# Performance work log

Measured on AMD Instinct MI355X. Metric: run time of the kernel, lower is better.

## Reference

```python
import jax, jax.numpy as jnp
from jax import lax
import numpy as np


def _farthest_point_sample(points, num_centroids):
    """points: [B, C, N] float. Returns int32 indices [B, num_centroids].

    Standard PointNet++ CUDA semantics: start from point index 0, maintain a
    running min squared distance to the selected set, pick argmax each step.
    """
    B, C, N = points.shape

    def step(carry, _):
        min_dist, farthest = carry  # [B, N], [B]
        # gather current centroid coords: [B, C, 1]
        centroid = jnp.take_along_axis(points, farthest[:, None, None], axis=2)
        d = jnp.sum((points - centroid) ** 2, axis=1)  # [B, N]
        min_dist = jnp.minimum(min_dist, d)
        nxt = jnp.argmax(min_dist, axis=1).astype(jnp.int32)  # [B]
        return (min_dist, nxt), farthest

    init = (jnp.full((B, N), jnp.finfo(points.dtype).max, points.dtype),
            jnp.zeros((B,), jnp.int32))
    _, idx = lax.scan(step, init, None, length=num_centroids)  # idx: [S, B]
    return idx.T  # [B, num_centroids]


def setup_inputs() -> dict:
    key = jax.random.key(0)
    B, C, N = 32, 3, 131072
    points = jax.random.normal(key, (B, C, N), dtype=jnp.float32)
    return {"points": points, "num_centroids": 2048}


def reference(points, num_centroids):
    return _farthest_point_sample(points, num_centroids)
```

## Files before the change

kernel.cpp:

```cpp
#include <hip/hip_runtime.h>
#include <stdint.h>

typedef unsigned long long u64;

#define NBATCH 32
#define NPTS   131072
#define KBLK   8
#define PPB    (NPTS / KBLK)
#define NTHR   1024
#define NWAVE  (NTHR / 64)
#define PPT    (PPB / NTHR)
#define FLT_MAX_C 3.402823466e+38f

__device__ __forceinline__ u64* slot_ptr(u64* slots, int b, int k, int par) {
    return slots + ((size_t)((b * KBLK + k) * 2 + par)) * 8;
}

__global__ __launch_bounds__(NTHR, 4)
void fps_kernel(const float* __restrict__ points, int* __restrict__ out,
                u64* __restrict__ slots, int S)
{
    const int b    = blockIdx.x & (NBATCH - 1);
    const int kk   = blockIdx.x >> 5;
    const int t    = threadIdx.x;
    const int lane = t & 63;
    const int wv   = t >> 6;

    const float* pb = points + (size_t)b * 3 * NPTS;
    const float* bx = pb + kk * PPB;
    const float* by = bx + NPTS;
    const float* bz = bx + 2 * NPTS;

    float px[PPT], py[PPT], pz[PPT], md[PPT];
    const int t4 = t * 4;
#pragma unroll
    for (int c = 0; c < PPT / 4; ++c) {
        float4 vx = *(const float4*)(bx + c * (NTHR * 4) + t4);
        float4 vy = *(const float4*)(by + c * (NTHR * 4) + t4);
        float4 vz = *(const float4*)(bz + c * (NTHR * 4) + t4);
        px[c*4+0]=vx.x; px[c*4+1]=vx.y; px[c*4+2]=vx.z; px[c*4+3]=vx.w;
        py[c*4+0]=vy.x; py[c*4+1]=vy.y; py[c*4+2]=vy.z; py[c*4+3]=vy.w;
        pz[c*4+0]=vz.x; pz[c*4+1]=vz.y; pz[c*4+2]=vz.z; pz[c*4+3]=vz.w;
        md[c*4+0]=FLT_MAX_C; md[c*4+1]=FLT_MAX_C;
        md[c*4+2]=FLT_MAX_C; md[c*4+3]=FLT_MAX_C;
    }

    __shared__ float s_v[NWAVE];
    __shared__ int   s_i[NWAVE];
    __shared__ int   s_bi;
    __shared__ unsigned s_bc[4];

    float cx = pb[0], cy = pb[NPTS], cz = pb[2 * NPTS];
    if (kk == 0 && t == 0) out[(size_t)b * S] = 0;

    for (int s = 1; s < S; ++s) {
        float bestv = -1.0f;
        int   bestp = 0;
#pragma unroll
        for (int p = 0; p < PPT; ++p) {
            float dx = __fsub_rn(px[p], cx);
            float dy = __fsub_rn(py[p], cy);
            float dz = __fsub_rn(pz[p], cz);
            float d  = __fadd_rn(__fadd_rn(__fmul_rn(dx, dx), __fmul_rn(dy, dy)),
                                 __fmul_rn(dz, dz));
            float m  = fminf(md[p], d);
            md[p] = m;
            bool tk = m > bestv;
            bestv = tk ? m : bestv;
            bestp = tk ? p : bestp;
        }
        int gidx = kk * PPB + (bestp >> 2) * (NTHR * 4) + t4 + (bestp & 3);

#pragma unroll
        for (int off = 32; off >= 1; off >>= 1) {
            float ov = __shfl_down(bestv, off);
            int   oi = __shfl_down(gidx, off);
            bool tk = (ov > bestv) || (ov == bestv && oi < gidx);
            bestv = tk ? ov : bestv;
            gidx  = tk ? oi : gidx;
        }
        if (lane == 0) { s_v[wv] = bestv; s_i[wv] = gidx; }
        __syncthreads();

        if (wv == 0) {
            float v16 = (lane < NWAVE) ? s_v[lane] : -1.0f;
            int   i16 = (lane < NWAVE) ? s_i[lane] : 0x7fffffff;
#pragma unroll
            for (int off = 8; off >= 1; off >>= 1) {
                float ov = __shfl_down(v16, off);
                int   oi = __shfl_down(i16, off);
                bool tk = (ov > v16) || (ov == v16 && oi < i16);
                v16 = tk ? ov : v16;
                i16 = tk ? oi : i16;
            }
            if (lane == 0) {
                u64 di = ((u64)(unsigned)s << 49)
                       | ((u64)__float_as_uint(v16) << 17)
                       | (u64)(unsigned)(131071 - i16);
                __hip_atomic_store(slot_ptr(slots, b, kk, s & 1) + 3, di,
                                   __ATOMIC_RELAXED, __HIP_MEMORY_SCOPE_AGENT);
                s_bi = i16;
            }
        }
        __syncthreads();

        int widx = s_bi;
        if ((widx >> 14) == kk) {
            int l = widx & (PPB - 1);
            if (t == ((l >> 2) & (NTHR - 1))) {
                int pw = ((l >> 12) << 2) | (l & 3);
                float wx = 0.f, wy = 0.f, wz = 0.f;
#pragma unroll
                for (int p = 0; p < PPT; ++p) {
                    bool e = (p == pw);
                    wx = e ? px[p] : wx; wy = e ? py[p] : wy; wz = e ? pz[p] : wz;
                }
                u64 tg = (u64)(unsigned)s << 32;
                u64* sp = slot_ptr(slots, b, kk, s & 1);
                __hip_atomic_store(sp + 0, tg | __float_as_uint(wx),
                                   __ATOMIC_RELAXED, __HIP_MEMORY_SCOPE_AGENT);
                __hip_atomic_store(sp + 1, tg | __float_as_uint(wy),
                                   __ATOMIC_RELAXED, __HIP_MEMORY_SCOPE_AGENT);
                __hip_atomic_store(sp + 2, tg | __float_as_uint(wz),
                                   __ATOMIC_RELAXED, __HIP_MEMORY_SCOPE_AGENT);
            }
        }

        if (wv == 0) {
            u64 got = 0;
            if (lane < 32) {
                u64* ps = slot_ptr(slots, b, lane >> 2, s & 1) + (lane & 3);
                const int sh = ((lane & 3) == 3) ? 49 : 32;
                do {
                    got = __hip_atomic_load(ps, __ATOMIC_RELAXED,
                                            __HIP_MEMORY_SCOPE_AGENT);
                } while ((int)(got >> sh) != s);
            }
            u64 dval = (u64)__shfl((long long)got, lane * 4 + 3);
            u64 dv = (lane < 8) ? dval : 0ull;
#pragma unroll
            for (int off = 4; off >= 1; off >>= 1) {
                u64 o = (u64)__shfl_down((long long)dv, off);
                dv = (o > dv) ? o : dv;
            }
            u64 win = (u64)__shfl((long long)dv, 0);
            u64 mask = __ballot(lane < 8 && dval == win);
            int w = __ffsll(mask) - 1;
            unsigned lo = (unsigned)got;
            unsigned cxb = (unsigned)__shfl((int)lo, w * 4 + 0);
            unsigned cyb = (unsigned)__shfl((int)lo, w * 4 + 1);
            unsigned czb = (unsigned)__shfl((int)lo, w * 4 + 2);
            int idx = 131071 - (int)(win & 0x1FFFF);
            if (lane == 0) {
                s_bc[0] = cxb; s_bc[1] = cyb; s_bc[2] = czb; s_bc[3] = (unsigned)idx;
                if (kk == 0) out[(size_t)b * S + s] = idx;
            }
        }
        __syncthreads();
        cx = __uint_as_float(s_bc[0]);
        cy = __uint_as_float(s_bc[1]);
        cz = __uint_as_float(s_bc[2]);
    }
}

extern "C" void kernel_launch(void* const* d_in, const int* in_sizes, int n_in,
                              void* d_out, int out_size, void* d_ws, size_t ws_size,
                              hipStream_t stream) {
    const float* points = (const float*)d_in[0];
    int* out   = (int*)d_out;
    u64* slots = (u64*)d_ws;
    int S = out_size / NBATCH;
    fps_kernel<<<dim3(NBATCH * KBLK), dim3(NTHR), 0, stream>>>(points, out, slots, S);
}
```

Before: 7.051 ms.

## Interleave two batches per block to hide cross-block sync latency

Each block now handles the same point slice for two batches (A and B), with the points split across 16 blocks per batch instead of 8. While one batch waits on the inter-block slot exchange, the block scans the other batch, and slot loads are prefetched ahead of polling. The goal is to hide the global-memory polling latency of the per-step all-to-all reduction. In exchange, register pressure stays similar per thread, each poll now covers 16 blocks, and the schedule becomes more intricate, including a tail step that finishes batch B alone.

Measured after the change: 10.42 ms. +47.8%, slower.

```diff
diff --git a/kernel.cpp b/kernel.cpp
--- a/kernel.cpp
+++ b/kernel.cpp
@@ -4,8 +4,9 @@
 typedef unsigned long long u64;
 
 #define NBATCH 32
+#define NPAIR  16
 #define NPTS   131072
-#define KBLK   8
+#define KBLK   16
 #define PPB    (NPTS / KBLK)
 #define NTHR   1024
 #define NWAVE  (NTHR / 64)
@@ -16,150 +17,230 @@
     return slots + ((size_t)((b * KBLK + k) * 2 + par)) * 8;
 }
 
+#define SCAN(PX,PY,PZ,MD,CX,CY,CZ,BV,GI) do {                                  \
+    float bv_ = -1.0f; int bp_ = 0;                                            \
+    _Pragma("unroll")                                                          \
+    for (int p = 0; p < PPT; ++p) {                                            \
+        float dx = __fsub_rn(PX[p], CX);                                       \
+        float dy = __fsub_rn(PY[p], CY);                                       \
+        float dz = __fsub_rn(PZ[p], CZ);                                       \
+        float d  = __fadd_rn(__fadd_rn(__fmul_rn(dx,dx), __fmul_rn(dy,dy)),    \
+                             __fmul_rn(dz,dz));                                \
+        float m  = fminf(MD[p], d);                                            \
+        MD[p] = m;                                                             \
+        bool tk = m > bv_;                                                     \
+        bv_ = tk ? m : bv_;                                                    \
+        bp_ = tk ? p : bp_;                                                    \
+    }                                                                          \
+    BV = bv_;                                                                  \
+    GI = kk * PPB + ((bp_ >> 2) * (NTHR * 4)) + t4 + (bp_ & 3);                \
+} while (0)
+
+#define REDPUB(PX,PY,PZ,BX,SS,BV,GI) do {                                      \
+    float bv_ = BV; int gi_ = GI;                                              \
+    _Pragma("unroll")                                                          \
+    for (int off = 32; off >= 1; off >>= 1) {                                  \
+        float ov = __shfl_down(bv_, off);                                      \
+        int   oi = __shfl_down(gi_, off);                                      \
+        bool tk = (ov > bv_) || (ov == bv_ && oi < gi_);                       \
+        bv_ = tk ? ov : bv_;                                                   \
+        gi_ = tk ? oi : gi_;                                                   \
+    }                                                                          \
+    if (lane == 0) { s_v[wv] = bv_; s_i[wv] = gi_; }                           \
+    __syncthreads();                                                           \
+    if (wv == 0) {                                                             \
+        float v16 = (lane < NWAVE) ? s_v[lane] : -1.0f;                        \
+        int   i16 = (lane < NWAVE) ? s_i[lane] : 0x7fffffff;                   \
+        _Pragma("unroll")                                                      \
+        for (int off = 8; off >= 1; off >>= 1) {                               \
+            float ov = __shfl_down(v16, off);                                  \
+            int   oi = __shfl_down(i16, off);                                  \
+            bool tk = (ov > v16) || (ov == v16 && oi < i16);                   \
+            v16 = tk ? ov : v16;                                               \
+            i16 = tk ? oi : i16;                                               \
+        }                                                                      \
+        if (lane == 0) {                                                       \
+            u64 di = ((u64)(unsigned)(SS) << 49)                               \
+                   | ((u64)__float_as_uint(v16) << 17)                         \
+                   | (u64)(unsigned)(131071 - i16);                            \
+            __hip_atomic_store(slot_ptr(slots, BX, kk, (SS) & 1) + 3, di,      \
+                               __ATOMIC_RELAXED, __HIP_MEMORY_SCOPE_AGENT);    \
+            s_bi = i16;                                                        \
+        }                                                                      \
+    }                                                                          \
+    __syncthreads();                                                           \
+    {                                                                          \
+        int widx = s_bi;                                                       \
+        if ((widx >> 13) == kk) {                                              \
+            int l = widx & (PPB - 1);                                          \
+            if (t == ((l >> 2) & (NTHR - 1))) {                                \
+                int pw = ((l >> 12) << 2) | (l & 3);                           \
+                float wx = 0.f, wy = 0.f, wz = 0.f;                            \
+                _Pragma("unroll")                                              \
+                for (int p = 0; p < PPT; ++p) {                                \
+                    bool e = (p == pw);                                        \
+                    wx = e ? PX[p] : wx;                                       \
+                    wy = e ? PY[p] : wy;                                       \
+                    wz = e ? PZ[p] : wz;                                       \
+                }                                                              \
+                u64 tg = (u64)(unsigned)(SS) << 32;                            \
+                u64* sp = slot_ptr(slots, BX, kk, (SS) & 1);                   \
+                __hip_atomic_store(sp + 0, tg | __float_as_uint(wx),           \
+                                   __ATOMIC_RELAXED, __HIP_MEMORY_SCOPE_AGENT);\
+                __hip_atomic_store(sp + 1, tg | __float_as_uint(wy),           \
+                                   __ATOMIC_RELAXED, __HIP_MEMORY_SCOPE_AGENT);\
+                __hip_atomic_store(sp + 2, tg | __float_as_uint(wz),           \
+                                   __ATOMIC_RELAXED, __HIP_MEMORY_SCOPE_AGENT);\
+            }                                                                  \
+        }                                                                      \
+    }                                                                          \
+} while (0)
+
+#define PREFETCH(BX, SS, PRE) do {                                             \
+    if (wv == 0) {                                                             \
+        u64* ps = slot_ptr(slots, BX, lane >> 2, (SS) & 1) + (lane & 3);       \
+        PRE = __hip_atomic_load(ps, __ATOMIC_RELAXED,                          \
+                                __HIP_MEMORY_SCOPE_AGENT);                     \
+    }                                                                          \
+} while (0)
+
+#define POLLSEL(BX, SS, PRE, SBC) do {                                         \
+    if (wv == 0) {                                                             \
+        u64* ps = slot_ptr(slots, BX, lane >> 2, (SS) & 1) + (lane & 3);       \
+        const int sh = ((lane & 3) == 3) ? 49 : 32;                            \
+        u64 got = PRE;                                                         \
+        while ((int)(got >> sh) != (SS))                                       \
+            got = __hip_atomic_load(ps, __ATOMIC_RELAXED,                      \
+                                    __HIP_MEMORY_SCOPE_AGENT);                 \
+        u64 dval = (u64)__shfl((long long)got, ((lane & 15) << 2) | 3);        \
+        u64 dv = (lane < 16) ? dval : 0ull;                                    \
+        _Pragma("unroll")                                                      \
+        for (int off = 8; off >= 1; off >>= 1) {                               \
+            u64 o = (u64)__shfl_down((long long)dv, off);                      \
+            dv = (o > dv) ? o : dv;                                            \
+        }                                                                      \
+        u64 win = (u64)__shfl((long long)dv, 0);                               \
+        u64 mask = __ballot(lane < 16 && dval == win);                         \
+        int w = __ffsll(mask) - 1;                                             \
+        unsigned lo = (unsigned)got;                                           \
+        unsigned cxb = (unsigned)__shfl((int)lo, (w << 2) | 0);                \
+        unsigned cyb = (unsigned)__shfl((int)lo, (w << 2) | 1);                \
+        unsigned czb = (unsigned)__shfl((int)lo, (w << 2) | 2);                \
+        int idx = 131071 - (int)(win & 0x1FFFF);                               \
+        if (lane == 0) {                                                       \
+            SBC[0] = cxb; SBC[1] = cyb; SBC[2] = czb;                          \
+            if (kk == 0) out[(size_t)(BX) * S + (SS)] = idx;                   \
+        }                                                                      \
+    }                                                                          \
+    __syncthreads();                                                           \
+} while (0)
+
 __global__ __launch_bounds__(NTHR, 4)
 void fps_kernel(const float* __restrict__ points, int* __restrict__ out,
                 u64* __restrict__ slots, int S)
 {
-    const int b    = blockIdx.x & (NBATCH - 1);
-    const int kk   = blockIdx.x >> 5;
+    const int pr   = blockIdx.x & (NPAIR - 1);
+    const int kk   = blockIdx.x >> 4;
+    const int bA   = pr;
+    const int bB   = pr + NPAIR;
     const int t    = threadIdx.x;
     const int lane = t & 63;
     const int wv   = t >> 6;
-
-    const float* pb = points + (size_t)b * 3 * NPTS;
-    const float* bx = pb + kk * PPB;
-    const float* by = bx + NPTS;
-    const float* bz = bx + 2 * NPTS;
-
-    float px[PPT], py[PPT], pz[PPT], md[PPT];
-    const int t4 = t * 4;
+    const int t4   = t * 4;
+
+    const float* pbA = points + (size_t)bA * 3 * NPTS;
+    const float* pbB = points + (size_t)bB * 3 * NPTS;
+    const float* bxA = pbA + kk * PPB;
+    const float* byA = bxA + NPTS;
+    const float* bzA = bxA + 2 * NPTS;
+    const float* bxB = pbB + kk * PPB;
+    const float* byB = bxB + NPTS;
+    const float* bzB = bxB + 2 * NPTS;
+
+    float pxA[PPT], pyA[PPT], pzA[PPT], mdA[PPT];
+    float pxB[PPT], pyB[PPT], pzB[PPT], mdB[PPT];
 #pragma unroll
     for (int c = 0; c < PPT / 4; ++c) {
-        float4 vx = *(const float4*)(bx + c * (NTHR * 4) + t4);
-        float4 vy = *(const float4*)(by + c * (NTHR * 4) + t4);
-        float4 vz = *(const float4*)(bz + c * (NTHR * 4) + t4);
-        px[c*4+0]=vx.x; px[c*4+1]=vx.y; px[c*4+2]=vx.z; px[c*4+3]=vx.w;
-        py[c*4+0]=vy.x; py[c*4+1]=vy.y; py[c*4+2]=vy.z; py[c*4+3]=vy.w;
-        pz[c*4+0]=vz.x; pz[c*4+1]=vz.y; pz[c*4+2]=vz.z; pz[c*4+3]=vz.w;
-        md[c*4+0]=FLT_MAX_C; md[c*4+1]=FLT_MAX_C;
-        md[c*4+2]=FLT_MAX_C; md[c*4+3]=FLT_MAX_C;
-    }
-
-    __shared__ float s_v[NWAVE];
-    __shared__ int   s_i[NWAVE];
-    __shared__ int   s_bi;
-    __shared__ unsigned s_bc[4];
-
-    float cx = pb[0], cy = pb[NPTS], cz = pb[2 * NPTS];
-    if (kk == 0 && t == 0) out[(size_t)b * S] = 0;
+        float4 vx = *(const float4*)(bxA + c * (NTHR * 4) + t4);
+        float4 vy = *(const float4*)(byA + c * (NTHR * 4) + t4);
+        float4 vz = *(const float4*)(bzA + c * (NTHR * 4) + t4);
+        pxA[c*4+0]=vx.x; pxA[c*4+1]=vx.y; pxA[c*4+2]=vx.z; pxA[c*4+3]=vx.w;
+        pyA[c*4+0]=vy.x; pyA[c*4+1]=vy.y; pyA[c*4+2]=vy.z; pyA[c*4+3]=vy.w;
+        pzA[c*4+0]=vz.x; pzA[c*4+1]=vz.y; pzA[c*4+2]=vz.z; pzA[c*4+3]=vz.w;
+        mdA[c*4+0]=FLT_MAX_C; mdA[c*4+1]=FLT_MAX_C;
+        mdA[c*4+2]=FLT_MAX_C; mdA[c*4+3]=FLT_MAX_C;
+    }
+#pragma unroll
+    for (int c = 0; c < PPT / 4; ++c) {
+        float4 vx = *(const float4*)(bxB + c * (NTHR * 4) + t4);
+        float4 vy = *(const float4*)(byB + c * (NTHR * 4) + t4);
+        float4 vz = *(const float4*)(bzB + c * (NTHR * 4) + t4);
+        pxB[c*4+0]=vx.x; pxB[c*4+1]=vx.y; pxB[c*4+2]=vx.z; pxB[c*4+3]=vx.w;
+        pyB[c*4+0]=vy.x; pyB[c*4+1]=vy.y; pyB[c*4+2]=vy.z; pyB[c*4+3]=vy.w;
+        pzB[c*4+0]=vz.x; pzB[c*4+1]=vz.y; pzB[c*4+2]=vz.z; pzB[c*4+3]=vz.w;
+        mdB[c*4+0]=FLT_MAX_C; mdB[c*4+1]=FLT_MAX_C;
+        mdB[c*4+2]=FLT_MAX_C; mdB[c*4+3]=FLT_MAX_C;
+    }
+
+    __shared__ float    s_v[NWAVE];
+    __shared__ int      s_i[NWAVE];
+    __shared__ int      s_bi;
+    __shared__ unsigned s_bcA[4];
+    __shared__ unsigned s_bcB[4];
+
+    float cxA = pbA[0], cyA = pbA[NPTS], czA = pbA[2 * NPTS];
+    float cxB = pbB[0], cyB = pbB[NPTS], czB = pbB[2 * NPTS];
+    if (kk == 0 && t == 0) {
+        out[(size_t)bA * S] = 0;
+        out[(size_t)bB * S] = 0;
+    }
+
+    u64 preA = 0, preB = 0;
+    float bv; int gi;
 
     for (int s = 1; s < S; ++s) {
-        float bestv = -1.0f;
-        int   bestp = 0;
-#pragma unroll
-        for (int p = 0; p < PPT; ++p) {
-            float dx = __fsub_rn(px[p], cx);
-            float dy = __fsub_rn(py[p], cy);
-            float dz = __fsub_rn(pz[p], cz);
-            float d  = __fadd_rn(__fadd_rn(__fmul_rn(dx, dx), __fmul_rn(dy, dy)),
-                                 __fmul_rn(dz, dz));
-            float m  = fminf(md[p], d);
-            md[p] = m;
-            bool tk = m > bestv;
-            bestv = tk ? m : bestv;
-            bestp = tk ? p : bestp;
+        SCAN(pxA, pyA, pzA, mdA, cxA, cyA, czA, bv, gi);
+        REDPUB(pxA, pyA, pzA, bA, s, bv, gi);
+
+        if (s >= 2) {
+            POLLSEL(bB, s - 1, preB, s_bcB);
+            cxB = __uint_as_float(s_bcB[0]);
+            cyB = __uint_as_float(s_bcB[1]);
+            czB = __uint_as_float(s_bcB[2]);
         }
-        int gidx = kk * PPB + (bestp >> 2) * (NTHR * 4) + t4 + (bestp & 3);
-
-#pragma unroll
-        for (int off = 32; off >= 1; off >>= 1) {
-            float ov = __shfl_down(bestv, off);
-            int   oi = __shfl_down(gidx, off);
-            bool tk = (ov > bestv) || (ov == bestv && oi < gidx);
-            bestv = tk ? ov : bestv;
-            gidx  = tk ? oi : gidx;
-        }
-        if (lane == 0) { s_v[wv] = bestv; s_i[wv] = gidx; }
-        __syncthreads();
-
+
+        SCAN(pxB, pyB, pzB, mdB, cxB, cyB, czB, bv, gi);
+        PREFETCH(bA, s, preA);
+        REDPUB(pxB, pyB, pzB, bB, s, bv, gi);
+
+        POLLSEL(bA, s, preA, s_bcA);
+        cxA = __uint_as_float(s_bcA[0]);
+        cyA = __uint_as_float(s_bcA[1]);
+        czA = __uint_as_float(s_bcA[2]);
+
+        PREFETCH(bB, s, preB);
+    }
+
+    {
+        const int ss = S - 1;
         if (wv == 0) {
-            float v16 = (lane < NWAVE) ? s_v[lane] : -1.0f;
-            int   i16 = (lane < NWAVE) ? s_i[lane] : 0x7fffffff;
+            u64* ps = slot_ptr(slots, bB, lane >> 2, ss & 1) + (lane & 3);
+            const int sh = ((lane & 3) == 3) ? 49 : 32;
+            u64 got = preB;
+            while ((int)(got >> sh) != ss)
+                got = __hip_atomic_load(ps, __ATOMIC_RELAXED,
+                                        __HIP_MEMORY_SCOPE_AGENT);
+            u64 dval = (u64)__shfl((long long)got, ((lane & 15) << 2) | 3);
+            u64 dv = (lane < 16) ? dval : 0ull;
 #pragma unroll
             for (int off = 8; off >= 1; off >>= 1) {
-                float ov = __shfl_down(v16, off);
-                int   oi = __shfl_down(i16, off);
-                bool tk = (ov > v16) || (ov == v16 && oi < i16);
-                v16 = tk ? ov : v16;
-                i16 = tk ? oi : i16;
-            }
-            if (lane == 0) {
-                u64 di = ((u64)(unsigned)s << 49)
-                       | ((u64)__float_as_uint(v16) << 17)
-                       | (u64)(unsigned)(131071 - i16);
-                __hip_atomic_store(slot_ptr(slots, b, kk, s & 1) + 3, di,
-                                   __ATOMIC_RELAXED, __HIP_MEMORY_SCOPE_AGENT);
-                s_bi = i16;
-            }
-        }
-        __syncthreads();
-
-        int widx = s_bi;
-        if ((widx >> 14) == kk) {
-            int l = widx & (PPB - 1);
-            if (t == ((l >> 2) & (NTHR - 1))) {
-                int pw = ((l >> 12) << 2) | (l & 3);
-                float wx = 0.f, wy = 0.f, wz = 0.f;
-#pragma unroll
-                for (int p = 0; p < PPT; ++p) {
-                    bool e = (p == pw);
-                    wx = e ? px[p] : wx; wy = e ? py[p] : wy; wz = e ? pz[p] : wz;
-                }
-                u64 tg = (u64)(unsigned)s << 32;
-                u64* sp = slot_ptr(slots, b, kk, s & 1);
-                __hip_atomic_store(sp + 0, tg | __float_as_uint(wx),
-                                   __ATOMIC_RELAXED, __HIP_MEMORY_SCOPE_AGENT);
-                __hip_atomic_store(sp + 1, tg | __float_as_uint(wy),
-                                   __ATOMIC_RELAXED, __HIP_MEMORY_SCOPE_AGENT);
-                __hip_atomic_store(sp + 2, tg | __float_as_uint(wz),
-                                   __ATOMIC_RELAXED, __HIP_MEMORY_SCOPE_AGENT);
-            }
-        }
-
-        if (wv == 0) {
-            u64 got = 0;
-            if (lane < 32) {
-                u64* ps = slot_ptr(slots, b, lane >> 2, s & 1) + (lane & 3);
-                const int sh = ((lane & 3) == 3) ? 49 : 32;
-                do {
-                    got = __hip_atomic_load(ps, __ATOMIC_RELAXED,
-                                            __HIP_MEMORY_SCOPE_AGENT);
-                } while ((int)(got >> sh) != s);
-            }
-            u64 dval = (u64)__shfl((long long)got, lane * 4 + 3);
-            u64 dv = (lane < 8) ? dval : 0ull;
-#pragma unroll
-            for (int off = 4; off >= 1; off >>= 1) {
                 u64 o = (u64)__shfl_down((long long)dv, off);
                 dv = (o > dv) ? o : dv;
             }
             u64 win = (u64)__shfl((long long)dv, 0);
-            u64 mask = __ballot(lane < 8 && dval == win);
-            int w = __ffsll(mask) - 1;
-            unsigned lo = (unsigned)got;
-            unsigned cxb = (unsigned)__shfl((int)lo, w * 4 + 0);
-            unsigned cyb = (unsigned)__shfl((int)lo, w * 4 + 1);
-            unsigned czb = (unsigned)__shfl((int)lo, w * 4 + 2);
             int idx = 131071 - (int)(win & 0x1FFFF);
-            if (lane == 0) {
-                s_bc[0] = cxb; s_bc[1] = cyb; s_bc[2] = czb; s_bc[3] = (unsigned)idx;
-                if (kk == 0) out[(size_t)b * S + s] = idx;
-            }
+            if (lane == 0 && kk == 0) out[(size_t)bB * S + ss] = idx;
         }
-        __syncthreads();
-        cx = __uint_as_float(s_bc[0]);
-        cy = __uint_as_float(s_bc[1]);
-        cz = __uint_as_float(s_bc[2]);
     }
 }
 
@@ -170,5 +251,5 @@
     int* out   = (int*)d_out;
     u64* slots = (u64*)d_ws;
     int S = out_size / NBATCH;
-    fps_kernel<<<dim3(NBATCH * KBLK), dim3(NTHR), 0, stream>>>(points, out, slots, S);
+    fps_kernel<<<dim3(NPAIR * KBLK), dim3(NTHR), 0, stream>>>(points, out, slots, S);
 }
```

## Fetch winner coords in wave reduction, drop a block barrier per step

Applied to the files above, without the earlier changes.

Each wave's winning lane now writes its packed key and coordinates to shared memory right after an xor-shuffle reduction. Wave 0 can then publish the block candidate's coords and key together and start polling the other blocks straight away. This removes one __syncthreads and the serialized owner-thread lookup from every FPS iteration, and the block's own slot is taken from registers instead of polled. The poll loop also issues the next load before checking the current one, to hide some of the latency of the cross-block handshake.

Result: slower. 7.674 ms (+8.8%).

```diff
diff --git a/kernel.cpp b/kernel.cpp
--- a/kernel.cpp
+++ b/kernel.cpp
@@ -45,9 +45,8 @@
         md[c*4+2]=FLT_MAX_C; md[c*4+3]=FLT_MAX_C;
     }
 
-    __shared__ float s_v[NWAVE];
-    __shared__ int   s_i[NWAVE];
-    __shared__ int   s_bi;
+    __shared__ u64      s_wk[NWAVE];
+    __shared__ unsigned s_wc[NWAVE][4];
     __shared__ unsigned s_bc[4];
 
     float cx = pb[0], cy = pb[NPTS], cz = pb[2 * NPTS];
@@ -71,88 +70,85 @@
         }
         int gidx = kk * PPB + (bestp >> 2) * (NTHR * 4) + t4 + (bestp & 3);
 
+        float wvv = bestv; int wvi = gidx;
 #pragma unroll
         for (int off = 32; off >= 1; off >>= 1) {
-            float ov = __shfl_down(bestv, off);
-            int   oi = __shfl_down(gidx, off);
-            bool tk = (ov > bestv) || (ov == bestv && oi < gidx);
-            bestv = tk ? ov : bestv;
-            gidx  = tk ? oi : gidx;
+            float ov = __shfl_xor(wvv, off);
+            int   oi = __shfl_xor(wvi, off);
+            bool tk = (ov > wvv) || (ov == wvv && oi < wvi);
+            wvv = tk ? ov : wvv;
+            wvi = tk ? oi : wvi;
         }
-        if (lane == 0) { s_v[wv] = bestv; s_i[wv] = gidx; }
+        if (bestv == wvv && gidx == wvi) {
+            float wx = 0.f, wy = 0.f, wz = 0.f;
+#pragma unroll
+            for (int p = 0; p < PPT; ++p) {
+                bool e = (p == bestp);
+                wx = e ? px[p] : wx; wy = e ? py[p] : wy; wz = e ? pz[p] : wz;
+            }
+            s_wk[wv] = ((u64)__float_as_uint(wvv) << 17)
+                     | (u64)(unsigned)(131071 - wvi);
+            s_wc[wv][0] = __float_as_uint(wx);
+            s_wc[wv][1] = __float_as_uint(wy);
+            s_wc[wv][2] = __float_as_uint(wz);
+        }
         __syncthreads();
 
         if (wv == 0) {
-            float v16 = (lane < NWAVE) ? s_v[lane] : -1.0f;
-            int   i16 = (lane < NWAVE) ? s_i[lane] : 0x7fffffff;
+            const int q = lane >> 2, r = lane & 3;
+            u64 orig = (lane < NWAVE) ? s_wk[lane] : 0ull;
+            u64 kmax = orig;
 #pragma unroll
             for (int off = 8; off >= 1; off >>= 1) {
-                float ov = __shfl_down(v16, off);
-                int   oi = __shfl_down(i16, off);
-                bool tk = (ov > v16) || (ov == v16 && oi < i16);
-                v16 = tk ? ov : v16;
-                i16 = tk ? oi : i16;
+                u64 o = (u64)__shfl_xor((long long)kmax, off);
+                kmax = (o > kmax) ? o : kmax;
             }
-            if (lane == 0) {
-                u64 di = ((u64)(unsigned)s << 49)
-                       | ((u64)__float_as_uint(v16) << 17)
-                       | (u64)(unsigned)(131071 - i16);
-                __hip_atomic_store(slot_ptr(slots, b, kk, s & 1) + 3, di,
+            u64 wmask = __ballot(lane < NWAVE && orig == kmax);
+            int wstar = __ffsll(wmask) - 1;
+
+            unsigned cb = s_wc[wstar][r];
+            u64 pubw = (r == 3)
+                ? (((u64)(unsigned)s << 49) | kmax)
+                : (((u64)(unsigned)s << 32) | (u64)cb);
+            if (lane < 4)
+                __hip_atomic_store(slot_ptr(slots, b, kk, s & 1) + r, pubw,
                                    __ATOMIC_RELAXED, __HIP_MEMORY_SCOPE_AGENT);
-                s_bi = i16;
+            u64 ownw = (u64)__shfl((long long)pubw, r);
+
+            u64 got = 0;
+            if (lane < 4 * KBLK && q != kk) {
+                u64* ps = slot_ptr(slots, b, q, s & 1) + r;
+                const int sh = (r == 3) ? 49 : 32;
+                u64 a  = __hip_atomic_load(ps, __ATOMIC_RELAXED,
+                                           __HIP_MEMORY_SCOPE_AGENT);
+                u64 nx = __hip_atomic_load(ps, __ATOMIC_RELAXED,
+                                           __HIP_MEMORY_SCOPE_AGENT);
+                while ((int)(a >> sh) != s) {
+                    a  = nx;
+                    nx = __hip_atomic_load(ps, __ATOMIC_RELAXED,
+                                           __HIP_MEMORY_SCOPE_AGENT);
+                }
+                got = a;
             }
-        }
-        __syncthreads();
+            if (q == kk) got = ownw;
 
-        int widx = s_bi;
-        if ((widx >> 14) == kk) {
-            int l = widx & (PPB - 1);
-            if (t == ((l >> 2) & (NTHR - 1))) {
-                int pw = ((l >> 12) << 2) | (l & 3);
-                float wx = 0.f, wy = 0.f, wz = 0.f;
-#pragma unroll
-                for (int p = 0; p < PPT; ++p) {
-                    bool e = (p == pw);
-                    wx = e ? px[p] : wx; wy = e ? py[p] : wy; wz = e ? pz[p] : wz;
-                }
-                u64 tg = (u64)(unsigned)s << 32;
-                u64* sp = slot_ptr(slots, b, kk, s & 1);
-                __hip_atomic_store(sp + 0, tg | __float_as_uint(wx),
-                                   __ATOMIC_RELAXED, __HIP_MEMORY_SCOPE_AGENT);
-                __hip_atomic_store(sp + 1, tg | __float_as_uint(wy),
-                                   __ATOMIC_RELAXED, __HIP_MEMORY_SCOPE_AGENT);
-                __hip_atomic_store(sp + 2, tg | __float_as_uint(wz),
-                                   __ATOMIC_RELAXED, __HIP_MEMORY_SCOPE_AGENT);
-            }
-        }
-
-        if (wv == 0) {
-            u64 got = 0;
-            if (lane < 32) {
-                u64* ps = slot_ptr(slots, b, lane >> 2, s & 1) + (lane & 3);
-                const int sh = ((lane & 3) == 3) ? 49 : 32;
-                do {
-                    got = __hip_atomic_load(ps, __ATOMIC_RELAXED,
-                                            __HIP_MEMORY_SCOPE_AGENT);
-                } while ((int)(got >> sh) != s);
-            }
-            u64 dval = (u64)__shfl((long long)got, lane * 4 + 3);
-            u64 dv = (lane < 8) ? dval : 0ull;
+            u64 dval = (u64)__shfl((long long)got, ((lane & 7) << 2) | 3);
+            u64 dv = (lane < KBLK) ? dval : 0ull;
 #pragma unroll
             for (int off = 4; off >= 1; off >>= 1) {
                 u64 o = (u64)__shfl_down((long long)dv, off);
                 dv = (o > dv) ? o : dv;
             }
             u64 win = (u64)__shfl((long long)dv, 0);
-            u64 mask = __ballot(lane < 8 && dval == win);
-            int w = __ffsll(mask) - 1;
+            u64 bmask = __ballot(lane < KBLK && dval == win);
+            int w = __ffsll(bmask) - 1;
             unsigned lo = (unsigned)got;
-            unsigned cxb = (unsigned)__shfl((int)lo, w * 4 + 0);
-            unsigned cyb = (unsigned)__shfl((int)lo, w * 4 + 1);
-            unsigned czb = (unsigned)__shfl((int)lo, w * 4 + 2);
+            unsigned cxb = (unsigned)__shfl((int)lo, (w << 2) | 0);
+            unsigned cyb = (unsigned)__shfl((int)lo, (w << 2) | 1);
+            unsigned czb = (unsigned)__shfl((int)lo, (w << 2) | 2);
             int idx = 131071 - (int)(win & 0x1FFFF);
             if (lane == 0) {
-                s_bc[0] = cxb; s_bc[1] = cyb; s_bc[2] = czb; s_bc[3] = (unsigned)idx;
+                s_bc[0] = cxb; s_bc[1] = cyb; s_bc[2] = czb;
                 if (kk == 0) out[(size_t)b * S + s] = idx;
             }
         }
```
